# Kernel optimization log

Hardware: AMD Instinct MI355X
Metric: run time of the kernel (lower is better)

The kernel has to match this reference:

```python
import jax, jax.numpy as jnp
import numpy as np

B, N, D = 8, 2048, 3
HIDDEN = (64, 128, 256)
LATENT = 128


def _layernorm(x, scale, bias, eps=1e-6):
    mu = jnp.mean(x, axis=-1, keepdims=True)
    var = jnp.mean((x - mu) ** 2, axis=-1, keepdims=True)
    return (x - mu) / jnp.sqrt(var + eps) * scale + bias


def setup_inputs() -> dict:
    key = jax.random.key(0)
    ks = jax.random.split(key, 8)
    inp = {
        "x": jax.random.normal(ks[0], (B, N, D), dtype=jnp.float32),
        "mask": jnp.ones((B, N), dtype=jnp.float32),
    }
    in_d = D
    for i, d in enumerate(HIDDEN):
        inp[f"W{i}"] = (jax.random.normal(ks[1 + i], (in_d, d), dtype=jnp.float32)
                        / np.float32(np.sqrt(in_d)))
        inp[f"b{i}"] = jnp.zeros((d,), dtype=jnp.float32)
        inp[f"g{i}"] = jnp.ones((d,), dtype=jnp.float32)
        inp[f"be{i}"] = jnp.zeros((d,), dtype=jnp.float32)
        in_d = d
    inp["Wz"] = (jax.random.normal(ks[5], (in_d, LATENT), dtype=jnp.float32)
                 / np.float32(np.sqrt(in_d)))
    inp["bz"] = jnp.zeros((LATENT,), dtype=jnp.float32)
    return inp


def reference(x, mask, W0, b0, g0, be0, W1, b1, g1, be1, W2, b2, g2, be2, Wz, bz):
    m = mask[..., None]                                   # (B, N, 1)
    count = jnp.sum(m, axis=1)                            # (B, 1)
    centroid = jnp.sum(x * m, axis=1, keepdims=True) / jnp.maximum(count, 1.0)[:, None, :]
    xc = x - centroid                                     # (B, N, D)

    # Pairwise squared distances; attention depends only on coordinates,
    # so it is identical for every layer -> compute once.
    diff = xc[:, :, None, :] - xc[:, None, :, :]          # (B, N, N, D)
    dist = jnp.sum(diff * diff, axis=-1)                  # (B, N, N)
    attn = jax.nn.softmax(-dist, axis=-1)                 # (B, N, N)

    h = xc
    for W, b, g, be in ((W0, b0, g0, be0), (W1, b1, g1, be1), (W2, b2, g2, be2)):
        h_agg = jnp.einsum('bij,bjd->bid', attn, h)       # weighted aggregation
        h = h_agg @ W + b
        h = _layernorm(h, g, be)
        h = jax.nn.swish(h)

    # Invariant readout: masked mean pool then Dense(latent)
    global_feat = jnp.sum(h * m, axis=1) / jnp.maximum(count, 1.0)
    z = global_feat @ Wz + bz                             # (B, latent)
    return z
```

## Files before the change

### kernel.cpp

```cpp
#include <hip/hip_runtime.h>
#include <hip/hip_bf16.h>

#define BATCH 8
#define NPTS 2048
#define LATENT 128

typedef __attribute__((ext_vector_type(8))) short short8;
typedef __attribute__((ext_vector_type(4))) float f32x4;

__device__ __forceinline__ ushort f2bf(float f) {
  unsigned int b = __float_as_uint(f);
  b += 0x7FFF + ((b >> 16) & 1);
  return (ushort)(b >> 16);
}
__device__ __forceinline__ float bf2f(ushort u) {
  return __uint_as_float(((unsigned int)u) << 16);
}
__device__ __forceinline__ unsigned int pkbf(float a, float b) {
  __hip_bfloat162 h = __float22bfloat162_rn(make_float2(a, b));
  return *(unsigned int*)&h;
}

typedef unsigned int __attribute__((address_space(1))) gas_uint;
typedef unsigned int __attribute__((address_space(3))) las_uint;
__device__ __forceinline__ void gl_lds16(const void* g, void* l) {
  __builtin_amdgcn_global_load_lds((const gas_uint*)g, (las_uint*)l, 16, 0, 0);
}

#define L2E 1.4426950408889634f
#define SC2 1.6986436f

__device__ __forceinline__ void wtrans_tile(const float* __restrict__ W,
    ushort* __restrict__ WT, int K, int N, int n0, int k0, int tid) {
  __shared__ ushort s[64][72];
  for (int i = tid; i < 64 * 64; i += 256) {
    const int kl = i >> 6, nl = i & 63;
    s[kl][nl] = f2bf(W[(size_t)(k0 + kl) * N + n0 + nl]);
  }
  __syncthreads();
  for (int i = tid; i < 64 * 64; i += 256) {
    const int nl = i >> 6, kl = i & 63;
    WT[(size_t)(n0 + nl) * K + k0 + kl] = s[kl][nl];
  }
}

__global__ __launch_bounds__(256) void setup_kernel(const float* __restrict__ x,
    const float* __restrict__ mask, float4* __restrict__ pnt,
    const float* __restrict__ W1, ushort* __restrict__ WT1,
    const float* __restrict__ W2, ushort* __restrict__ WT2,
    const float* __restrict__ Wz, ushort* __restrict__ WzT) {
  const int bid = blockIdx.x;
  const int tid = threadIdx.x;
  if (bid >= 8) {
    if (bid < 10) wtrans_tile(W1, WT1, 64, 128, (bid - 8) * 64, 0, tid);
    else if (bid < 18) {
      const int idx = bid - 10;
      wtrans_tile(W2, WT2, 128, 256, (idx & 3) * 64, (idx >> 2) * 64, tid);
    } else {
      const int idx = bid - 18;
      wtrans_tile(Wz, WzT, 256, 128, (idx & 1) * 64, (idx >> 1) * 64, tid);
    }
    return;
  }
  const int b = bid;
  const float* xb = x + (size_t)b * NPTS * 3;
  const float* mb = mask + (size_t)b * NPTS;
  float s0 = 0.f, s1 = 0.f, s2 = 0.f, c = 0.f;
  for (int n = tid; n < NPTS; n += 256) {
    float m = mb[n];
    s0 += xb[n * 3 + 0] * m;
    s1 += xb[n * 3 + 1] * m;
    s2 += xb[n * 3 + 2] * m;
    c += m;
  }
  __shared__ float red[4][256];
  red[0][tid] = s0; red[1][tid] = s1; red[2][tid] = s2; red[3][tid] = c;
  __syncthreads();
  for (int off = 128; off > 0; off >>= 1) {
    if (tid < off) {
      red[0][tid] += red[0][tid + off];
      red[1][tid] += red[1][tid + off];
      red[2][tid] += red[2][tid + off];
      red[3][tid] += red[3][tid + off];
    }
    __syncthreads();
  }
  const float cnt = fmaxf(red[3][0], 1.0f);
  const float c0 = red[0][0] / cnt, c1 = red[1][0] / cnt, c2 = red[2][0] / cnt;
  float4* pb = pnt + (size_t)b * NPTS;
  for (int n = tid; n < NPTS; n += 256) {
    const float a0 = xb[n * 3 + 0] - c0;
    const float a1 = xb[n * 3 + 1] - c1;
    const float a2 = xb[n * 3 + 2] - c2;
    pb[n] = make_float4(a0 * SC2, a1 * SC2, a2 * SC2,
                        -(a0 * a0 + a1 * a1 + a2 * a2) * L2E);
  }
}

__global__ __launch_bounds__(512) void layer0_kernel(
    const float4* __restrict__ pnt, const float* __restrict__ W,
    const float* __restrict__ bias, const float* __restrict__ g,
    const float* __restrict__ be, ushort* __restrict__ hout) {
  const int b = blockIdx.y;
  const int i0 = blockIdx.x * 64;
  const int tid = threadIdx.x;
  const int il = tid & 63, part = tid >> 6;
  const float4* pb = pnt + (size_t)b * NPTS;
  const float4 pi = pb[i0 + il];
  float a0 = 0.f, a1 = 0.f, a2 = 0.f, dn = 0.f;
#pragma unroll 8
  for (int j = part * 256; j < part * 256 + 256; j++) {
    const float4 pj = pb[j];
    float arg = pi.w + pj.w;
    arg = fmaf(pi.x, pj.x, arg);
    arg = fmaf(pi.y, pj.y, arg);
    arg = fmaf(pi.z, pj.z, arg);
    const float w = __builtin_amdgcn_exp2f(arg);
    a0 = fmaf(w, pj.x, a0);
    a1 = fmaf(w, pj.y, a1);
    a2 = fmaf(w, pj.z, a2);
    dn += w;
  }
  __shared__ float4 sred[8][64];
  __shared__ float srow[64 * 3];
  __shared__ ushort lt[64][64];
  sred[part][il] = make_float4(a0, a1, a2, dn);
  __syncthreads();
  if (tid < 64) {
    float A0 = 0.f, A1 = 0.f, A2 = 0.f, DN = 0.f;
#pragma unroll
    for (int p = 0; p < 8; p++) {
      const float4 r = sred[p][tid];
      A0 += r.x; A1 += r.y; A2 += r.z; DN += r.w;
    }
    const float inv = 1.0f / (DN * SC2);
    srow[tid * 3 + 0] = A0 * inv;
    srow[tid * 3 + 1] = A1 * inv;
    srow[tid * 3 + 2] = A2 * inv;
  }
  __syncthreads();
  const int wv = tid >> 6, lane = tid & 63;
  const float w0c = W[lane], w1c = W[64 + lane], w2c = W[128 + lane];
  const float gv = g[lane], bev = be[lane], bv = bias[lane];
#pragma unroll
  for (int r = 0; r < 8; r++) {
    const int row = wv * 8 + r;
    float o = bv;
    o = fmaf(srow[row * 3 + 0], w0c, o);
    o = fmaf(srow[row * 3 + 1], w1c, o);
    o = fmaf(srow[row * 3 + 2], w2c, o);
    float m1 = o, m2 = o * o;
#pragma unroll
    for (int off = 32; off > 0; off >>= 1) {
      m1 += __shfl_xor(m1, off, 64);
      m2 += __shfl_xor(m2, off, 64);
    }
    const float mu = m1 / 64.f;
    const float rstd = rsqrtf(m2 / 64.f - mu * mu + 1e-6f);
    const float v = (o - mu) * rstd * gv + bev;
    const float act = v / (1.0f + __expf(-v));
    lt[row][lane] = f2bf(act);
  }
  __syncthreads();
  if (tid < 64) {
    ushort tmp[64];
#pragma unroll
    for (int r = 0; r < 64; r++) tmp[r] = lt[r][tid];
    ushort* dst = hout + ((size_t)b * 64 + tid) * NPTS + i0;
#pragma unroll
    for (int c = 0; c < 8; c++)
      *(uint4*)(dst + c * 8) = *(uint4*)&tmp[c * 8];
  }
}

template <int DIN, int DOUT, bool POOL, int MINW>
__global__ __launch_bounds__(256, MINW) void fused_layer(
    const float4* __restrict__ pnt, const ushort* __restrict__ hT,
    const ushort* __restrict__ WT, const float* __restrict__ bias,
    const float* __restrict__ g, const float* __restrict__ be,
    ushort* __restrict__ hout, const float* __restrict__ mask,
    float* __restrict__ partial) {
  constexpr int NT = DIN / 16;
  constexpr int HALF = NPTS / 2;
  constexpr int TILES = HALF / 64;
  constexpr int NCOL = DOUT / 32;
  constexpr int PS = DIN + 8;
  constexpr int PN = DIN + 4;
  constexpr int SHT_B = 2 * 2 * DIN * 64 * 2;
  constexpr int SPNT_B = 2 * 2 * 64 * 16;
  constexpr int LOOP_B = SHT_B + SPNT_B;
  constexpr int SNUM_B = 32 * PN * 4;
  constexpr int OFF_SROW = SNUM_B;
  constexpr int OFF_SDEN = OFF_SROW + 32 * PS * 2;
  constexpr int OFF_SINV = OFF_SDEN + 128;
  constexpr int OFF_SSTAT = OFF_SINV + 128;
  constexpr int EPI_B = OFF_SSTAT + 512;
  constexpr int SMEM_B = LOOP_B > EPI_B ? LOOP_B : EPI_B;
  __shared__ __align__(16) char smem[SMEM_B];
  ushort* sht = (ushort*)smem;
  float4* spnt = (float4*)(smem + SHT_B);

  const int b = blockIdx.y;
  const int i0 = blockIdx.x * 32;
  const int tid = threadIdx.x;
  const int wv = tid >> 6, lane = tid & 63;
  const int h = wv >> 1;
  const int u = wv & 1;
  const int m = lane & 15, q = lane >> 4;
  const float4* pb = pnt + (size_t)b * NPTS;
  const ushort* hb = hT + (size_t)b * DIN * NPTS;

  const float4 pi0 = pb[i0 + m];
  const float4 pi1 = pb[i0 + 16 + m];

  f32x4 acc0[NT], acc1[NT];
#pragma unroll
  for (int nt = 0; nt < NT; nt++)
#pragma unroll
    for (int e = 0; e < 4; e++) { acc0[nt][e] = 0.f; acc1[nt][e] = 0.f; }
  float dacc0 = 0.f, dacc1 = 0.f;

  constexpr int NCH = DIN / 16;
  const int srow8 = lane >> 3;
  const int scsrc = (lane & 7) ^ srow8;
  const int jsw = ((lane & 7) << 3) | (lane >> 3);

  auto stage = [&](int t, int bf) {
    const int jb = t * 64;
#pragma unroll
    for (int i = 0; i < NCH; i++) {
      const int idx = wv * NCH + i;
      const int h2 = idx / (DIN / 8);
      const int oct = idx % (DIN / 8);
      const int row = oct * 8 + srow8;
      gl_lds16(hb + (size_t)row * NPTS + h2 * HALF + jb + scsrc * 8,
               sht + ((size_t)(bf * 2 + h2) * DIN + oct * 8) * 64);
    }
    if (wv == 0) {
#pragma unroll
      for (int h2 = 0; h2 < 2; h2++)
        gl_lds16(pb + h2 * HALF + jb + jsw, spnt + (bf * 2 + h2) * 64);
    }
  };

  stage(0, 0);
  __syncthreads();
  for (int t = 0; t < TILES; t++) {
    const int bf = t & 1;
    if (t + 1 < TILES) stage(t + 1, bf ^ 1);
    float w0a[8], w1a[8];
#pragma unroll
    for (int jj = 0; jj < 8; jj++) {
      const float4 pj = spnt[(bf * 2 + h) * 64 + ((jj << 3) | (u * 4 + q))];
      float a0 = pi0.w + pj.w;
      a0 = fmaf(pi0.x, pj.x, a0);
      a0 = fmaf(pi0.y, pj.y, a0);
      a0 = fmaf(pi0.z, pj.z, a0);
      float a1 = pi1.w + pj.w;
      a1 = fmaf(pi1.x, pj.x, a1);
      a1 = fmaf(pi1.y, pj.y, a1);
      a1 = fmaf(pi1.z, pj.z, a1);
      w0a[jj] = __builtin_amdgcn_exp2f(a0);
      w1a[jj] = __builtin_amdgcn_exp2f(a1);
      dacc0 += w0a[jj]; dacc1 += w1a[jj];
    }
    unsigned int au0[4], au1[4];
#pragma unroll
    for (int p = 0; p < 4; p++) {
      au0[p] = pkbf(w0a[2 * p], w0a[2 * p + 1]);
      au1[p] = pkbf(w1a[2 * p], w1a[2 * p + 1]);
    }
    const short8 af0 = *(short8*)au0;
    const short8 af1 = *(short8*)au1;
#pragma unroll
    for (int nt = 0; nt < NT; nt++) {
      const int d = nt * 16 + m;
      const short8 bfr = *(const short8*)
          &sht[((size_t)(bf * 2 + h) * DIN + d) * 64 + (((u * 4 + q) ^ (m & 7)) << 3)];
      acc0[nt] = __builtin_amdgcn_mfma_f32_16x16x32_bf16(af0, bfr, acc0[nt], 0, 0, 0);
      acc1[nt] = __builtin_amdgcn_mfma_f32_16x16x32_bf16(af1, bfr, acc1[nt], 0, 0, 0);
    }
    __syncthreads();
  }

  float* snum = (float*)smem;
  ushort* srow = (ushort*)(smem + OFF_SROW);
  float* sden = (float*)(smem + OFF_SDEN);
  float* sinv = (float*)(smem + OFF_SINV);
  float* sstat = (float*)(smem + OFF_SSTAT);

  dacc0 += __shfl_xor(dacc0, 16, 64);
  dacc0 += __shfl_xor(dacc0, 32, 64);
  dacc1 += __shfl_xor(dacc1, 16, 64);
  dacc1 += __shfl_xor(dacc1, 32, 64);
  for (int p = 0; p < 4; p++) {
    if (wv == p) {
      if (p == 0) {
#pragma unroll
        for (int nt = 0; nt < NT; nt++)
#pragma unroll
          for (int r = 0; r < 4; r++) {
            snum[(q * 4 + r) * PN + nt * 16 + m] = acc0[nt][r];
            snum[(16 + q * 4 + r) * PN + nt * 16 + m] = acc1[nt][r];
          }
        if (q == 0) { sden[m] = dacc0; sden[16 + m] = dacc1; }
      } else {
#pragma unroll
        for (int nt = 0; nt < NT; nt++)
#pragma unroll
          for (int r = 0; r < 4; r++) {
            snum[(q * 4 + r) * PN + nt * 16 + m] += acc0[nt][r];
            snum[(16 + q * 4 + r) * PN + nt * 16 + m] += acc1[nt][r];
          }
        if (q == 0) { sden[m] += dacc0; sden[16 + m] += dacc1; }
      }
    }
    __syncthreads();
  }
  if (tid < 32) sinv[tid] = 1.0f / sden[tid];
  __syncthreads();
  for (int idx = tid; idx < 32 * (DIN / 2); idx += 256) {
    const int r = idx / (DIN / 2), c2 = idx % (DIN / 2);
    const float v0 = snum[r * PN + 2 * c2] * sinv[r];
    const float v1 = snum[r * PN + 2 * c2 + 1] * sinv[r];
    *(unsigned int*)&srow[r * PS + 2 * c2] = pkbf(v0, v1);
  }
  __syncthreads();

  const int rg2 = wv >> 1, ch = wv & 1;
  short8 afrag[DIN / 32];
#pragma unroll
  for (int kt = 0; kt < DIN / 32; kt++)
    afrag[kt] = *(const short8*)&srow[(rg2 * 16 + m) * PS + kt * 32 + q * 8];
  f32x4 oacc[NCOL];
#pragma unroll
  for (int c = 0; c < NCOL; c++)
#pragma unroll
    for (int e = 0; e < 4; e++) oacc[c][e] = 0.f;
#pragma unroll
  for (int c = 0; c < NCOL; c++) {
    const int n0 = (ch * NCOL + c) * 16;
#pragma unroll
    for (int kt = 0; kt < DIN / 32; kt++) {
      const short8 bfrag = *(const short8*)(WT + (size_t)(n0 + m) * DIN + kt * 32 + q * 8);
      oacc[c] = __builtin_amdgcn_mfma_f32_16x16x32_bf16(afrag[kt], bfrag, oacc[c], 0, 0, 0);
    }
  }

  float bcol[NCOL];
#pragma unroll
  for (int c = 0; c < NCOL; c++) bcol[c] = bias[(ch * NCOL + c) * 16 + m];
#pragma unroll
  for (int r = 0; r < 4; r++) {
    float m1 = 0.f, m2 = 0.f;
#pragma unroll
    for (int c = 0; c < NCOL; c++) {
      const float v = oacc[c][r] + bcol[c];
      m1 += v; m2 += v * v;
    }
#pragma unroll
    for (int off = 8; off > 0; off >>= 1) {
      m1 += __shfl_xor(m1, off, 64);
      m2 += __shfl_xor(m2, off, 64);
    }
    if (m == 0) {
      const int row = rg2 * 16 + q * 4 + r;
      sstat[(row * 2 + ch) * 2 + 0] = m1;
      sstat[(row * 2 + ch) * 2 + 1] = m2;
    }
  }
  __syncthreads();

  ushort* lt = (ushort*)smem;
  float* sp = (float*)smem;
  float pacc[NCOL];
  if (POOL) {
#pragma unroll
    for (int c = 0; c < NCOL; c++) pacc[c] = 0.f;
  }
#pragma unroll
  for (int r = 0; r < 4; r++) {
    const int row = rg2 * 16 + q * 4 + r;
    const float m1 = sstat[(row * 2 + 0) * 2 + 0] + sstat[(row * 2 + 1) * 2 + 0];
    const float m2 = sstat[(row * 2 + 0) * 2 + 1] + sstat[(row * 2 + 1) * 2 + 1];
    const float mu = m1 / DOUT;
    const float rstd = rsqrtf(m2 / DOUT - mu * mu + 1e-6f);
    float mval = 0.f;
    if (POOL) mval = mask[(size_t)b * NPTS + i0 + row];
#pragma unroll
    for (int c = 0; c < NCOL; c++) {
      const int dco = (ch * NCOL + c) * 16 + m;
      const float v = (oacc[c][r] + bcol[c] - mu) * rstd * g[dco] + be[dco];
      const float act = v / (1.0f + __expf(-v));
      if (POOL) pacc[c] = fmaf(act, mval, pacc[c]);
      else lt[row * DOUT + dco] = f2bf(act);
    }
  }
  if (POOL) {
#pragma unroll
    for (int c = 0; c < NCOL; c++) {
      float v = pacc[c];
      v += __shfl_xor(v, 16, 64);
      v += __shfl_xor(v, 32, 64);
      if (q == 0) sp[rg2 * DOUT + (ch * NCOL + c) * 16 + m] = v;
    }
    __syncthreads();
    if (tid < DOUT)
      partial[((size_t)b * (NPTS / 32) + blockIdx.x) * DOUT + tid] =
          sp[tid] + sp[DOUT + tid];
  } else {
    __syncthreads();
    if (tid < DOUT) {
      ushort tmp[32];
#pragma unroll
      for (int r = 0; r < 32; r++) tmp[r] = lt[r * DOUT + tid];
      ushort* dst = hout + ((size_t)b * DOUT + tid) * NPTS + i0;
#pragma unroll
      for (int c = 0; c < 4; c++)
        *(uint4*)(dst + c * 8) = *(uint4*)&tmp[c * 8];
    }
  }
}

__global__ __launch_bounds__(256) void readout_kernel(
    const float* __restrict__ partial, const float* __restrict__ mask,
    const ushort* __restrict__ WzT, const float* __restrict__ bz,
    float* __restrict__ out) {
  const int b = blockIdx.x;
  const int tid = threadIdx.x;
  const float* pb = partial + (size_t)b * (NPTS / 32) * 256;
  float s0 = 0.f, s1 = 0.f, s2 = 0.f, s3 = 0.f;
#pragma unroll 4
  for (int p = 0; p < NPTS / 32; p += 4) {
    s0 += pb[(size_t)(p + 0) * 256 + tid];
    s1 += pb[(size_t)(p + 1) * 256 + tid];
    s2 += pb[(size_t)(p + 2) * 256 + tid];
    s3 += pb[(size_t)(p + 3) * 256 + tid];
  }
  const float s = (s0 + s1) + (s2 + s3);
  const float* mb = mask + (size_t)b * NPTS;
  float c = 0.f;
  for (int n = tid; n < NPTS; n += 256) c += mb[n];
  __shared__ float red[256];
  red[tid] = c;
  __syncthreads();
  for (int off = 128; off > 0; off >>= 1) {
    if (tid < off) red[tid] += red[tid + off];
    __syncthreads();
  }
  const float cnt = fmaxf(red[0], 1.0f);
  __shared__ float gf[256];
  gf[tid] = s / cnt;
  __syncthreads();
  const int col = tid & 127, part = tid >> 7;
  float z = 0.f;
  const ushort* wr = WzT + (size_t)col * 256 + part * 128;
  const float* gp = gf + part * 128;
#pragma unroll 4
  for (int d = 0; d < 128; d += 8) {
    const short8 w8 = *(const short8*)(wr + d);
#pragma unroll
    for (int e = 0; e < 8; e++)
      z = fmaf(gp[d + e], bf2f((ushort)w8[e]), z);
  }
  __shared__ float zred[256];
  zred[tid] = z;
  __syncthreads();
  if (tid < LATENT)
    out[(size_t)b * LATENT + tid] = bz[tid] + zred[tid] + zred[128 + tid];
}

extern "C" void kernel_launch(void* const* d_in, const int* in_sizes, int n_in,
                              void* d_out, int out_size, void* d_ws, size_t ws_size,
                              hipStream_t stream) {
  const float* x    = (const float*)d_in[0];
  const float* mask = (const float*)d_in[1];
  const float* W0   = (const float*)d_in[2];
  const float* b0   = (const float*)d_in[3];
  const float* g0   = (const float*)d_in[4];
  const float* be0  = (const float*)d_in[5];
  const float* W1   = (const float*)d_in[6];
  const float* b1   = (const float*)d_in[7];
  const float* g1   = (const float*)d_in[8];
  const float* be1  = (const float*)d_in[9];
  const float* W2   = (const float*)d_in[10];
  const float* b2   = (const float*)d_in[11];
  const float* g2   = (const float*)d_in[12];
  const float* be2  = (const float*)d_in[13];
  const float* Wz   = (const float*)d_in[14];
  const float* bz   = (const float*)d_in[15];
  float* out = (float*)d_out;

  char* ws = (char*)d_ws;
  float4* pnt     = (float4*)(ws);
  ushort* h1T     = (ushort*)(ws + 262144);
  ushort* h2T     = (ushort*)(ws + 2359296);
  float*  partial = (float*)(ws + 6553600);
  ushort* WT1     = (ushort*)(ws + 7077888);
  ushort* WT2     = (ushort*)(ws + 7094272);
  ushort* WzT     = (ushort*)(ws + 7159808);

  setup_kernel<<<dim3(26), dim3(256), 0, stream>>>(
      x, mask, pnt, W1, WT1, W2, WT2, Wz, WzT);

  layer0_kernel<<<dim3(NPTS / 64, BATCH), dim3(512), 0, stream>>>(
      pnt, W0, b0, g0, be0, h1T);

  fused_layer<64, 128, false, 4><<<dim3(NPTS / 32, BATCH), dim3(256), 0, stream>>>(
      pnt, h1T, WT1, b1, g1, be1, h2T, nullptr, nullptr);

  fused_layer<128, 256, true, 2><<<dim3(NPTS / 32, BATCH), dim3(256), 0, stream>>>(
      pnt, h2T, WT2, b2, g2, be2, nullptr, mask, partial);

  readout_kernel<<<dim3(BATCH), dim3(256), 0, stream>>>(partial, mask, WzT, bz, out);
}
```

Measured before the change: 175.1 us.

## Load h fragments directly from global into registers, preload all points into LDS

Replaces the double-buffered global-to-LDS staging of the feature tiles with direct per-wave global loads of MFMA B fragments into registers. Each wave now covers a quarter of the j range instead of a half. All 2048 point coordinates are loaded once into LDS with a swizzled layout, and the per-tile barriers are removed. The second fused layer's min-waves bound rises from 2 to 3. This trades LDS traffic and barriers for uncoalesced, latency-exposed global loads with no software prefetch, and the larger point array (32KB) raises LDS use.

Measured after the change: 187.5 us. 7.1% more time.

```diff
diff --git a/kernel.cpp b/kernel.cpp
--- a/kernel.cpp
+++ b/kernel.cpp
@@ -19,12 +19,6 @@
 __device__ __forceinline__ unsigned int pkbf(float a, float b) {
   __hip_bfloat162 h = __float22bfloat162_rn(make_float2(a, b));
   return *(unsigned int*)&h;
-}
-
-typedef unsigned int __attribute__((address_space(1))) gas_uint;
-typedef unsigned int __attribute__((address_space(3))) las_uint;
-__device__ __forceinline__ void gl_lds16(const void* g, void* l) {
-  __builtin_amdgcn_global_load_lds((const gas_uint*)g, (las_uint*)l, 16, 0, 0);
 }
 
 #define L2E 1.4426950408889634f
@@ -181,37 +175,39 @@
     ushort* __restrict__ hout, const float* __restrict__ mask,
     float* __restrict__ partial) {
   constexpr int NT = DIN / 16;
-  constexpr int HALF = NPTS / 2;
-  constexpr int TILES = HALF / 64;
+  constexpr int QJ = NPTS / 4;
+  constexpr int KS = QJ / 32;
   constexpr int NCOL = DOUT / 32;
   constexpr int PS = DIN + 8;
   constexpr int PN = DIN + 4;
-  constexpr int SHT_B = 2 * 2 * DIN * 64 * 2;
-  constexpr int SPNT_B = 2 * 2 * 64 * 16;
-  constexpr int LOOP_B = SHT_B + SPNT_B;
+  constexpr int SPNT_B = NPTS * 16;
   constexpr int SNUM_B = 32 * PN * 4;
   constexpr int OFF_SROW = SNUM_B;
   constexpr int OFF_SDEN = OFF_SROW + 32 * PS * 2;
   constexpr int OFF_SINV = OFF_SDEN + 128;
   constexpr int OFF_SSTAT = OFF_SINV + 128;
   constexpr int EPI_B = OFF_SSTAT + 512;
-  constexpr int SMEM_B = LOOP_B > EPI_B ? LOOP_B : EPI_B;
+  constexpr int SMEM_B = SPNT_B > EPI_B ? SPNT_B : EPI_B;
   __shared__ __align__(16) char smem[SMEM_B];
-  ushort* sht = (ushort*)smem;
-  float4* spnt = (float4*)(smem + SHT_B);
+  float4* sp = (float4*)smem;
 
   const int b = blockIdx.y;
   const int i0 = blockIdx.x * 32;
   const int tid = threadIdx.x;
   const int wv = tid >> 6, lane = tid & 63;
-  const int h = wv >> 1;
-  const int u = wv & 1;
   const int m = lane & 15, q = lane >> 4;
   const float4* pb = pnt + (size_t)b * NPTS;
   const ushort* hb = hT + (size_t)b * DIN * NPTS;
 
+#pragma unroll
+  for (int i = 0; i < NPTS / 256; i++) {
+    const int j = i * 256 + tid;
+    const int phys = (j & ~31) | (((j & 7) << 2) | ((j >> 3) & 3));
+    sp[phys] = pb[j];
+  }
   const float4 pi0 = pb[i0 + m];
   const float4 pi1 = pb[i0 + 16 + m];
+  __syncthreads();
 
   f32x4 acc0[NT], acc1[NT];
 #pragma unroll
@@ -220,38 +216,18 @@
     for (int e = 0; e < 4; e++) { acc0[nt][e] = 0.f; acc1[nt][e] = 0.f; }
   float dacc0 = 0.f, dacc1 = 0.f;
 
-  constexpr int NCH = DIN / 16;
-  const int srow8 = lane >> 3;
-  const int scsrc = (lane & 7) ^ srow8;
-  const int jsw = ((lane & 7) << 3) | (lane >> 3);
-
-  auto stage = [&](int t, int bf) {
-    const int jb = t * 64;
-#pragma unroll
-    for (int i = 0; i < NCH; i++) {
-      const int idx = wv * NCH + i;
-      const int h2 = idx / (DIN / 8);
-      const int oct = idx % (DIN / 8);
-      const int row = oct * 8 + srow8;
-      gl_lds16(hb + (size_t)row * NPTS + h2 * HALF + jb + scsrc * 8,
-               sht + ((size_t)(bf * 2 + h2) * DIN + oct * 8) * 64);
-    }
-    if (wv == 0) {
-#pragma unroll
-      for (int h2 = 0; h2 < 2; h2++)
-        gl_lds16(pb + h2 * HALF + jb + jsw, spnt + (bf * 2 + h2) * 64);
-    }
-  };
-
-  stage(0, 0);
-  __syncthreads();
-  for (int t = 0; t < TILES; t++) {
-    const int bf = t & 1;
-    if (t + 1 < TILES) stage(t + 1, bf ^ 1);
+  const int jq = wv * QJ;
+
+  for (int k = 0; k < KS; k++) {
+    const int j0 = jq + k * 32;
+    short8 bq[NT];
+#pragma unroll
+    for (int nt = 0; nt < NT; nt++)
+      bq[nt] = *(const short8*)(hb + (size_t)(nt * 16 + m) * NPTS + j0 + q * 8);
     float w0a[8], w1a[8];
 #pragma unroll
     for (int jj = 0; jj < 8; jj++) {
-      const float4 pj = spnt[(bf * 2 + h) * 64 + ((jj << 3) | (u * 4 + q))];
+      const float4 pj = sp[j0 + ((jj << 2) | q)];
       float a0 = pi0.w + pj.w;
       a0 = fmaf(pi0.x, pj.x, a0);
       a0 = fmaf(pi0.y, pj.y, a0);
@@ -274,14 +250,11 @@
     const short8 af1 = *(short8*)au1;
 #pragma unroll
     for (int nt = 0; nt < NT; nt++) {
-      const int d = nt * 16 + m;
-      const short8 bfr = *(const short8*)
-          &sht[((size_t)(bf * 2 + h) * DIN + d) * 64 + (((u * 4 + q) ^ (m & 7)) << 3)];
-      acc0[nt] = __builtin_amdgcn_mfma_f32_16x16x32_bf16(af0, bfr, acc0[nt], 0, 0, 0);
-      acc1[nt] = __builtin_amdgcn_mfma_f32_16x16x32_bf16(af1, bfr, acc1[nt], 0, 0, 0);
-    }
-    __syncthreads();
-  }
+      acc0[nt] = __builtin_amdgcn_mfma_f32_16x16x32_bf16(af0, bq[nt], acc0[nt], 0, 0, 0);
+      acc1[nt] = __builtin_amdgcn_mfma_f32_16x16x32_bf16(af1, bq[nt], acc1[nt], 0, 0, 0);
+    }
+  }
+  __syncthreads();
 
   float* snum = (float*)smem;
   ushort* srow = (ushort*)(smem + OFF_SROW);
@@ -372,7 +345,7 @@
   __syncthreads();
 
   ushort* lt = (ushort*)smem;
-  float* sp = (float*)smem;
+  float* spl = (float*)smem;
   float pacc[NCOL];
   if (POOL) {
 #pragma unroll
@@ -402,12 +375,12 @@
       float v = pacc[c];
       v += __shfl_xor(v, 16, 64);
       v += __shfl_xor(v, 32, 64);
-      if (q == 0) sp[rg2 * DOUT + (ch * NCOL + c) * 16 + m] = v;
+      if (q == 0) spl[rg2 * DOUT + (ch * NCOL + c) * 16 + m] = v;
     }
     __syncthreads();
     if (tid < DOUT)
       partial[((size_t)b * (NPTS / 32) + blockIdx.x) * DOUT + tid] =
-          sp[tid] + sp[DOUT + tid];
+          spl[tid] + spl[DOUT + tid];
   } else {
     __syncthreads();
     if (tid < DOUT) {
@@ -509,7 +482,7 @@
   fused_layer<64, 128, false, 4><<<dim3(NPTS / 32, BATCH), dim3(256), 0, stream>>>(
       pnt, h1T, WT1, b1, g1, be1, h2T, nullptr, nullptr);
 
-  fused_layer<128, 256, true, 2><<<dim3(NPTS / 32, BATCH), dim3(256), 0, stream>>>(
+  fused_layer<128, 256, true, 3><<<dim3(NPTS / 32, BATCH), dim3(256), 0, stream>>>(
       pnt, h2T, WT2, b2, g2, be2, nullptr, mask, partial);
 
   readout_kernel<<<dim3(BATCH), dim3(256), 0, stream>>>(partial, mask, WzT, bz, out);
```

## Use 64-row, 512-thread fused kernel for the final attention layer

Applied to the files above, without the earlier changes.

Adds a new fused attention+dense+layernorm+pool kernel that processes 64 query rows per block with 8 waves instead of 32 rows with 4 waves, and uses it for the 128->256 layer. Each staged key tile of h and points is now reused by twice as many query rows, halving global/LDS staging traffic per row. The split-key partial sums are reduced across four wave groups through shared memory with serialized syncs. The pooled partial buffer shrinks and the readout loop and workspace offsets are adjusted to match. The trade-off is fewer blocks (256 total) and higher register and LDS pressure per block.

Measured after the change: 183.3 us. +4.7%, slower.

```diff
diff --git a/kernel.cpp b/kernel.cpp
--- a/kernel.cpp
+++ b/kernel.cpp
@@ -173,8 +173,267 @@
   }
 }
 
+template <int DIN, int DOUT, bool POOL>
+__global__ __launch_bounds__(512, 2) void fused_v5(
+    const float4* __restrict__ pnt, const ushort* __restrict__ hT,
+    const ushort* __restrict__ WT, const float* __restrict__ bias,
+    const float* __restrict__ g, const float* __restrict__ be,
+    ushort* __restrict__ hout, const float* __restrict__ mask,
+    float* __restrict__ partial) {
+  constexpr int NT = DIN / 16;
+  constexpr int HALF = NPTS / 2;
+  constexpr int TILES = HALF / 64;
+  constexpr int NCOL = DOUT / 32;
+  constexpr int PS = DIN + 8;
+  constexpr int PN = DIN + 4;
+  constexpr int SHT_B = 2 * 2 * DIN * 64 * 2;
+  constexpr int SPNT_B = 2 * 2 * 64 * 16;
+  constexpr int LOOP_B = SHT_B + SPNT_B;
+  constexpr int SNUM_B = 64 * PN * 4;
+  constexpr int OFF_SROW = SNUM_B;
+  constexpr int OFF_SDEN = OFF_SROW + 64 * PS * 2;
+  constexpr int OFF_SINV = OFF_SDEN + 256;
+  constexpr int OFF_SSTAT = OFF_SINV + 256;
+  constexpr int EPI_B = OFF_SSTAT + 1024;
+  constexpr int SMEM_B = LOOP_B > EPI_B ? LOOP_B : EPI_B;
+  __shared__ __align__(16) char smem[SMEM_B];
+  ushort* sht = (ushort*)smem;
+  float4* spnt = (float4*)(smem + SHT_B);
+
+  const int b = blockIdx.y;
+  const int i0 = blockIdx.x * 64;
+  const int tid = threadIdx.x;
+  const int wv = tid >> 6, lane = tid & 63;
+  const int h = (wv >> 1) & 1;
+  const int u = wv & 1;
+  const int rg = wv >> 2;
+  const int m = lane & 15, q = lane >> 4;
+  const float4* pb = pnt + (size_t)b * NPTS;
+  const ushort* hb = hT + (size_t)b * DIN * NPTS;
+
+  const float4 pi0 = pb[i0 + rg * 32 + m];
+  const float4 pi1 = pb[i0 + rg * 32 + 16 + m];
+
+  f32x4 acc0[NT], acc1[NT];
+#pragma unroll
+  for (int nt = 0; nt < NT; nt++)
+#pragma unroll
+    for (int e = 0; e < 4; e++) { acc0[nt][e] = 0.f; acc1[nt][e] = 0.f; }
+  float dacc0 = 0.f, dacc1 = 0.f;
+
+  constexpr int NCH = DIN / 32;
+  const int srow8 = lane >> 3;
+  const int scsrc = (lane & 7) ^ srow8;
+  const int jsw = ((lane & 7) << 3) | (lane >> 3);
+
+  auto stage = [&](int t, int bf) {
+    const int jb = t * 64;
+#pragma unroll
+    for (int i = 0; i < NCH; i++) {
+      const int idx = wv * NCH + i;
+      const int h2 = idx / (DIN / 8);
+      const int oct = idx % (DIN / 8);
+      const int row = oct * 8 + srow8;
+      gl_lds16(hb + (size_t)row * NPTS + h2 * HALF + jb + scsrc * 8,
+               sht + ((size_t)(bf * 2 + h2) * DIN + oct * 8) * 64);
+    }
+    if (wv == 0) {
+#pragma unroll
+      for (int h2 = 0; h2 < 2; h2++)
+        gl_lds16(pb + h2 * HALF + jb + jsw, spnt + (bf * 2 + h2) * 64);
+    }
+  };
+
+  stage(0, 0);
+  __syncthreads();
+  for (int t = 0; t < TILES; t++) {
+    const int bf = t & 1;
+    if (t + 1 < TILES) stage(t + 1, bf ^ 1);
+    unsigned int au0[4], au1[4];
+#pragma unroll
+    for (int p = 0; p < 4; p++) {
+      float wp[4];
+#pragma unroll
+      for (int e = 0; e < 2; e++) {
+        const int jj = 2 * p + e;
+        const float4 pj = spnt[(bf * 2 + h) * 64 + ((jj << 3) | (u * 4 + q))];
+        float a0 = pi0.w + pj.w;
+        a0 = fmaf(pi0.x, pj.x, a0);
+        a0 = fmaf(pi0.y, pj.y, a0);
+        a0 = fmaf(pi0.z, pj.z, a0);
+        float a1 = pi1.w + pj.w;
+        a1 = fmaf(pi1.x, pj.x, a1);
+        a1 = fmaf(pi1.y, pj.y, a1);
+        a1 = fmaf(pi1.z, pj.z, a1);
+        wp[e] = __builtin_amdgcn_exp2f(a0);
+        wp[2 + e] = __builtin_amdgcn_exp2f(a1);
+      }
+      dacc0 += wp[0] + wp[1];
+      dacc1 += wp[2] + wp[3];
+      au0[p] = pkbf(wp[0], wp[1]);
+      au1[p] = pkbf(wp[2], wp[3]);
+    }
+    const short8 af0 = *(short8*)au0;
+    const short8 af1 = *(short8*)au1;
+#pragma unroll
+    for (int nt = 0; nt < NT; nt++) {
+      const int d = nt * 16 + m;
+      const short8 bfr = *(const short8*)
+          &sht[((size_t)(bf * 2 + h) * DIN + d) * 64 + (((u * 4 + q) ^ (m & 7)) << 3)];
+      acc0[nt] = __builtin_amdgcn_mfma_f32_16x16x32_bf16(af0, bfr, acc0[nt], 0, 0, 0);
+      acc1[nt] = __builtin_amdgcn_mfma_f32_16x16x32_bf16(af1, bfr, acc1[nt], 0, 0, 0);
+    }
+    __syncthreads();
+  }
+
+  float* snum = (float*)smem;
+  ushort* srow = (ushort*)(smem + OFF_SROW);
+  float* sden = (float*)(smem + OFF_SDEN);
+  float* sinv = (float*)(smem + OFF_SINV);
+  float* sstat = (float*)(smem + OFF_SSTAT);
+
+  dacc0 += __shfl_xor(dacc0, 16, 64);
+  dacc0 += __shfl_xor(dacc0, 32, 64);
+  dacc1 += __shfl_xor(dacc1, 16, 64);
+  dacc1 += __shfl_xor(dacc1, 32, 64);
+  const int quarter = wv & 3;
+  for (int p = 0; p < 4; p++) {
+    if (quarter == p) {
+      if (p == 0) {
+#pragma unroll
+        for (int nt = 0; nt < NT; nt++)
+#pragma unroll
+          for (int r = 0; r < 4; r++) {
+            snum[(rg * 32 + q * 4 + r) * PN + nt * 16 + m] = acc0[nt][r];
+            snum[(rg * 32 + 16 + q * 4 + r) * PN + nt * 16 + m] = acc1[nt][r];
+          }
+        if (q == 0) {
+          sden[rg * 32 + m] = dacc0;
+          sden[rg * 32 + 16 + m] = dacc1;
+        }
+      } else {
+#pragma unroll
+        for (int nt = 0; nt < NT; nt++)
+#pragma unroll
+          for (int r = 0; r < 4; r++) {
+            snum[(rg * 32 + q * 4 + r) * PN + nt * 16 + m] += acc0[nt][r];
+            snum[(rg * 32 + 16 + q * 4 + r) * PN + nt * 16 + m] += acc1[nt][r];
+          }
+        if (q == 0) {
+          sden[rg * 32 + m] += dacc0;
+          sden[rg * 32 + 16 + m] += dacc1;
+        }
+      }
+    }
+    __syncthreads();
+  }
+  if (tid < 64) sinv[tid] = 1.0f / sden[tid];
+  __syncthreads();
+  for (int idx = tid; idx < 64 * (DIN / 2); idx += 512) {
+    const int r = idx / (DIN / 2), c2 = idx % (DIN / 2);
+    const float v0 = snum[r * PN + 2 * c2] * sinv[r];
+    const float v1 = snum[r * PN + 2 * c2 + 1] * sinv[r];
+    *(unsigned int*)&srow[r * PS + 2 * c2] = pkbf(v0, v1);
+  }
+  __syncthreads();
+
+  const int rg2 = wv >> 1, ch = wv & 1;
+  short8 afrag[DIN / 32];
+#pragma unroll
+  for (int kt = 0; kt < DIN / 32; kt++)
+    afrag[kt] = *(const short8*)&srow[(rg2 * 16 + m) * PS + kt * 32 + q * 8];
+  f32x4 oacc[NCOL];
+#pragma unroll
+  for (int c = 0; c < NCOL; c++)
+#pragma unroll
+    for (int e = 0; e < 4; e++) oacc[c][e] = 0.f;
+#pragma unroll
+  for (int c = 0; c < NCOL; c++) {
+    const int n0 = (ch * NCOL + c) * 16;
+#pragma unroll
+    for (int kt = 0; kt < DIN / 32; kt++) {
+      const short8 bfrag = *(const short8*)(WT + (size_t)(n0 + m) * DIN + kt * 32 + q * 8);
+      oacc[c] = __builtin_amdgcn_mfma_f32_16x16x32_bf16(afrag[kt], bfrag, oacc[c], 0, 0, 0);
+    }
+  }
+
+  float bcol[NCOL];
+#pragma unroll
+  for (int c = 0; c < NCOL; c++) bcol[c] = bias[(ch * NCOL + c) * 16 + m];
+#pragma unroll
+  for (int r = 0; r < 4; r++) {
+    float m1 = 0.f, m2 = 0.f;
+#pragma unroll
+    for (int c = 0; c < NCOL; c++) {
+      const float v = oacc[c][r] + bcol[c];
+      m1 += v; m2 += v * v;
+    }
+#pragma unroll
+    for (int off = 8; off > 0; off >>= 1) {
+      m1 += __shfl_xor(m1, off, 64);
+      m2 += __shfl_xor(m2, off, 64);
+    }
+    if (m == 0) {
+      const int row = rg2 * 16 + q * 4 + r;
+      sstat[(row * 2 + ch) * 2 + 0] = m1;
+      sstat[(row * 2 + ch) * 2 + 1] = m2;
+    }
+  }
+  __syncthreads();
+
+  ushort* lt = (ushort*)smem;
+  float* spl = (float*)smem;
+  float pacc[NCOL];
+  if (POOL) {
+#pragma unroll
+    for (int c = 0; c < NCOL; c++) pacc[c] = 0.f;
+  }
+#pragma unroll
+  for (int r = 0; r < 4; r++) {
+    const int row = rg2 * 16 + q * 4 + r;
+    const float m1 = sstat[(row * 2 + 0) * 2 + 0] + sstat[(row * 2 + 1) * 2 + 0];
+    const float m2 = sstat[(row * 2 + 0) * 2 + 1] + sstat[(row * 2 + 1) * 2 + 1];
+    const float mu = m1 / DOUT;
+    const float rstd = rsqrtf(m2 / DOUT - mu * mu + 1e-6f);
+    float mval = 0.f;
+    if (POOL) mval = mask[(size_t)b * NPTS + i0 + row];
+#pragma unroll
+    for (int c = 0; c < NCOL; c++) {
+      const int dco = (ch * NCOL + c) * 16 + m;
+      const float v = (oacc[c][r] + bcol[c] - mu) * rstd * g[dco] + be[dco];
+      const float act = v / (1.0f + __expf(-v));
+      if (POOL) pacc[c] = fmaf(act, mval, pacc[c]);
+      else lt[row * DOUT + dco] = f2bf(act);
+    }
+  }
+  if (POOL) {
+#pragma unroll
+    for (int c = 0; c < NCOL; c++) {
+      float v = pacc[c];
+      v += __shfl_xor(v, 16, 64);
+      v += __shfl_xor(v, 32, 64);
+      if (q == 0) spl[rg2 * DOUT + (ch * NCOL + c) * 16 + m] = v;
+    }
+    __syncthreads();
+    if (tid < DOUT)
+      partial[((size_t)b * (NPTS / 64) + blockIdx.x) * DOUT + tid] =
+          (spl[tid] + spl[DOUT + tid]) + (spl[2 * DOUT + tid] + spl[3 * DOUT + tid]);
+  } else {
+    __syncthreads();
+    if (tid < DOUT) {
+      ushort tmp[64];
+#pragma unroll
+      for (int r = 0; r < 64; r++) tmp[r] = lt[r * DOUT + tid];
+      ushort* dst = hout + ((size_t)b * DOUT + tid) * NPTS + i0;
+#pragma unroll
+      for (int c = 0; c < 8; c++)
+        *(uint4*)(dst + c * 8) = *(uint4*)&tmp[c * 8];
+    }
+  }
+}
+
 template <int DIN, int DOUT, bool POOL, int MINW>
-__global__ __launch_bounds__(256, MINW) void fused_layer(
+__global__ __launch_bounds__(256, MINW) void fused_v6(
     const float4* __restrict__ pnt, const ushort* __restrict__ hT,
     const ushort* __restrict__ WT, const float* __restrict__ bias,
     const float* __restrict__ g, const float* __restrict__ be,
@@ -372,7 +631,7 @@
   __syncthreads();
 
   ushort* lt = (ushort*)smem;
-  float* sp = (float*)smem;
+  float* spl = (float*)smem;
   float pacc[NCOL];
   if (POOL) {
 #pragma unroll
@@ -402,12 +661,12 @@
       float v = pacc[c];
       v += __shfl_xor(v, 16, 64);
       v += __shfl_xor(v, 32, 64);
-      if (q == 0) sp[rg2 * DOUT + (ch * NCOL + c) * 16 + m] = v;
+      if (q == 0) spl[rg2 * DOUT + (ch * NCOL + c) * 16 + m] = v;
     }
     __syncthreads();
     if (tid < DOUT)
       partial[((size_t)b * (NPTS / 32) + blockIdx.x) * DOUT + tid] =
-          sp[tid] + sp[DOUT + tid];
+          spl[tid] + spl[DOUT + tid];
   } else {
     __syncthreads();
     if (tid < DOUT) {
@@ -428,10 +687,10 @@
     float* __restrict__ out) {
   const int b = blockIdx.x;
   const int tid = threadIdx.x;
-  const float* pb = partial + (size_t)b * (NPTS / 32) * 256;
+  const float* pb = partial + (size_t)b * (NPTS / 64) * 256;
   float s0 = 0.f, s1 = 0.f, s2 = 0.f, s3 = 0.f;
-#pragma unroll 4
-  for (int p = 0; p < NPTS / 32; p += 4) {
+#pragma unroll
+  for (int p = 0; p < NPTS / 64; p += 4) {
     s0 += pb[(size_t)(p + 0) * 256 + tid];
     s1 += pb[(size_t)(p + 1) * 256 + tid];
     s2 += pb[(size_t)(p + 2) * 256 + tid];
@@ -496,9 +755,9 @@
   ushort* h1T     = (ushort*)(ws + 262144);
   ushort* h2T     = (ushort*)(ws + 2359296);
   float*  partial = (float*)(ws + 6553600);
-  ushort* WT1     = (ushort*)(ws + 7077888);
-  ushort* WT2     = (ushort*)(ws + 7094272);
-  ushort* WzT     = (ushort*)(ws + 7159808);
+  ushort* WT1     = (ushort*)(ws + 6815744);
+  ushort* WT2     = (ushort*)(ws + 6832128);
+  ushort* WzT     = (ushort*)(ws + 6897664);
 
   setup_kernel<<<dim3(26), dim3(256), 0, stream>>>(
       x, mask, pnt, W1, WT1, W2, WT2, Wz, WzT);
@@ -506,10 +765,10 @@
   layer0_kernel<<<dim3(NPTS / 64, BATCH), dim3(512), 0, stream>>>(
       pnt, W0, b0, g0, be0, h1T);
 
-  fused_layer<64, 128, false, 4><<<dim3(NPTS / 32, BATCH), dim3(256), 0, stream>>>(
+  fused_v6<64, 128, false, 4><<<dim3(NPTS / 32, BATCH), dim3(256), 0, stream>>>(
       pnt, h1T, WT1, b1, g1, be1, h2T, nullptr, nullptr);
 
-  fused_layer<128, 256, true, 2><<<dim3(NPTS / 32, BATCH), dim3(256), 0, stream>>>(
+  fused_v5<128, 256, true><<<dim3(NPTS / 64, BATCH), dim3(512), 0, stream>>>(
       pnt, h2T, WT2, b2, g2, be2, nullptr, mask, partial);
 
   readout_kernel<<<dim3(BATCH), dim3(256), 0, stream>>>(partial, mask, WzT, bz, out);
```
